# Performance work log

Hardware: AMD Instinct MI355X
Metric: run time of the kernel (lower is better)

Reference implementation:

```python
import jax, jax.numpy as jnp
import numpy as np

ALPHA = 0.2  # LeakyReLU negative slope

def setup_inputs() -> dict:
    key = jax.random.key(0)
    k1, k2, k3 = jax.random.split(key, 3)
    B, N, IN_DIM = 16, 1024, 128
    HEADS, HEAD_DIM = 2, 64  # out_dim = 128
    h = jax.random.normal(k1, (B, N, IN_DIM), dtype=jnp.float32)
    # xavier_uniform with gain=1.414 ~ uniform(-b, b); exact init unimportant for correctness
    bW = 1.414 * np.sqrt(6.0 / (IN_DIM + HEAD_DIM))
    W = jax.random.uniform(k2, (HEADS, IN_DIM, HEAD_DIM), minval=-bW, maxval=bW, dtype=jnp.float32)
    ba = 1.414 * np.sqrt(6.0 / (2 * HEAD_DIM + 1))
    a = jax.random.uniform(k3, (HEADS, 2 * HEAD_DIM, 1), minval=-ba, maxval=ba, dtype=jnp.float32)
    return {"h": h, "W": W, "a": a}

def reference(h, W, a):
    B, N, in_dim = h.shape
    heads, _, head_dim = W.shape
    out_dim = heads * head_dim
    # h_prime: [B, N, H, D]
    hp = jnp.einsum('bni,hio->bnho', h, W)
    # Split additive attention: a . [h_i ; h_j] = a_src . h_i + a_dst . h_j (same math as concat)
    a_src = a[:, :head_dim, 0]   # [H, D]
    a_dst = a[:, head_dim:, 0]   # [H, D]
    e_src = jnp.einsum('bnhd,hd->bhn', hp, a_src)  # [B, H, N]
    e_dst = jnp.einsum('bmhd,hd->bhm', hp, a_dst)  # [B, H, N]
    e = e_src[:, :, :, None] + e_dst[:, :, None, :]  # [B, H, N, N]
    e = jnp.where(e >= 0, e, ALPHA * e)  # LeakyReLU(0.2)
    att = jax.nn.softmax(e, axis=-1)
    # dropout p=0.0 (eval-deterministic): no-op
    h_new = jnp.einsum('bhnm,bmho->bnho', att, hp).reshape(B, N, out_dim)
    out = h_new + h if in_dim == out_dim else h_new
    return jax.nn.elu(out)
```

## Files before the change

kernel.cpp:

```cpp
#include <hip/hip_runtime.h>
#include <math.h>


#define LOG2E 1.44269504088896340736f

typedef __bf16 bf16x8 __attribute__((ext_vector_type(8)));
typedef float floatx4 __attribute__((ext_vector_type(4)));

union U16x8 { uint4 u; bf16x8 b; };

__device__ __forceinline__ unsigned short f2bf(float f) {
    union { __bf16 b; unsigned short u; } x;
    x.b = (__bf16)f;
    return x.u;
}

__global__ __launch_bounds__(256) void gat_prep(
    const float* __restrict__ Wg,
    const float* __restrict__ ag,
    unsigned short* __restrict__ Wp,
    float* __restrict__ acat)
{
    const int t = threadIdx.x;
    const int base = blockIdx.x * 1024;
#pragma unroll
    for (int i = 0; i < 4; ++i) {
        int idx = base + i * 256 + t;
        int c = idx & 127, k = idx >> 7;
        float v = Wg[(c >> 6) * 8192 + k * 64 + (c & 63)];
        Wp[((k >> 3) * 128 + c) * 8 + (k & 7)] = f2bf(v);
    }
    if (blockIdx.x == 0 && t < 128) {
        acat[t]       = ag[(t >> 6) * 128 + (t & 63)];
        acat[128 + t] = ag[(t >> 6) * 128 + 64 + (t & 63)];
    }
}

__global__ __launch_bounds__(256) void gat_hp(
    const float* __restrict__ hg,
    const unsigned short* __restrict__ Wp,
    const float* __restrict__ acat,
    unsigned short* __restrict__ hpB,
    float* __restrict__ es_g,
    float* __restrict__ ed_g)
{
    const int t = threadIdx.x;
    const int lane = t & 63;
    const int wv = blockIdx.x * 4 + (t >> 6);
    const int rt = wv >> 1;
    const int half = wv & 1;
    const int n0 = rt * 16;
    const int col = lane & 15, quad = lane >> 4;

    floatx4 acc[4];
#pragma unroll
    for (int ct = 0; ct < 4; ++ct) acc[ct] = (floatx4){0.f, 0.f, 0.f, 0.f};

    const float* hrow = hg + (size_t)(n0 + col) * 128;
    const uint4* wp4 = (const uint4*)Wp;
#pragma unroll
    for (int kq = 0; kq < 4; ++kq) {
        float4 h0 = *(const float4*)(hrow + kq * 32 + quad * 8);
        float4 h1 = *(const float4*)(hrow + kq * 32 + quad * 8 + 4);
        bf16x8 af;
        af[0] = (__bf16)h0.x; af[1] = (__bf16)h0.y;
        af[2] = (__bf16)h0.z; af[3] = (__bf16)h0.w;
        af[4] = (__bf16)h1.x; af[5] = (__bf16)h1.y;
        af[6] = (__bf16)h1.z; af[7] = (__bf16)h1.w;
        const uint4* wbase = wp4 + (size_t)(kq * 4 + quad) * 128 + half * 64;
#pragma unroll
        for (int ct = 0; ct < 4; ++ct) {
            U16x8 bu; bu.u = wbase[ct * 16 + col];
            acc[ct] = __builtin_amdgcn_mfma_f32_16x16x32_bf16(af, bu.b, acc[ct], 0, 0, 0);
        }
    }

    const int b = n0 >> 10;
    const int nloc = n0 & 1023;
    const int bh = b * 2 + half;

    float esr[4] = {0.f, 0.f, 0.f, 0.f}, edr[4] = {0.f, 0.f, 0.f, 0.f};
#pragma unroll
    for (int ct = 0; ct < 4; ++ct) {
        int c = half * 64 + ct * 16 + col;
        float as = acat[c], ad = acat[128 + c];
#pragma unroll
        for (int r = 0; r < 4; ++r) {
            esr[r] = fmaf(acc[ct][r], as, esr[r]);
            edr[r] = fmaf(acc[ct][r], ad, edr[r]);
        }
    }
#pragma unroll
    for (int off = 1; off <= 8; off <<= 1) {
#pragma unroll
        for (int r = 0; r < 4; ++r) {
            esr[r] += __shfl_xor(esr[r], off, 64);
            edr[r] += __shfl_xor(edr[r], off, 64);
        }
    }
    if (col == 0) {
        size_t base = (size_t)bh * 1024 + nloc + quad * 4;
#pragma unroll
        for (int r = 0; r < 4; ++r) {
            es_g[base + r] = esr[r];
            ed_g[base + r] = edr[r];
        }
    }

    const int gloc = (nloc >> 3) + (quad >> 1);
#pragma unroll
    for (int ct = 0; ct < 4; ++ct) {
        int d = ct * 16 + col;
        uint2 pk;
        pk.x = (unsigned)f2bf(acc[ct][0]) | ((unsigned)f2bf(acc[ct][1]) << 16);
        pk.y = (unsigned)f2bf(acc[ct][2]) | ((unsigned)f2bf(acc[ct][3]) << 16);
        size_t idx = ((size_t)(bh * 128 + gloc) * 64 + d) * 8 + (quad & 1) * 4;
        *(uint2*)(hpB + idx) = pk;
    }
}

__global__ __launch_bounds__(256, 4) void gat_attn(
    const float* __restrict__ hg,
    const unsigned short* __restrict__ hpB,
    const float* __restrict__ es_g,
    const float* __restrict__ ed_g,
    float* __restrict__ out)
{
    __shared__ float red[4 * 64 * 17];

    const int t = threadIdx.x;
    const int lane = t & 63;
    const int w = t >> 6;
    const int bh = blockIdx.x & 31;
    const int nt = blockIdx.x >> 5;
    const int b = bh >> 1, hh = bh & 1;
    const int n0 = nt * 16;
    const int col = lane & 15, quad = lane >> 4;

    const float* edrow = ed_g + (size_t)bh * 1024;

    float mx = -1e30f;
#pragma unroll
    for (int i = 0; i < 4; ++i) {
        float4 v = *(const float4*)(edrow + lane * 16 + i * 4);
        mx = fmaxf(mx, fmaxf(fmaxf(v.x, v.y), fmaxf(v.z, v.w)));
    }
#pragma unroll
    for (int off = 1; off < 64; off <<= 1) mx = fmaxf(mx, __shfl_xor(mx, off, 64));

    const float s2 = es_g[(size_t)bh * 1024 + n0 + col] * LOG2E;
    const float x0 = s2 + mx * LOG2E;
    const float M = fmaxf(x0, 0.2f * x0);
    const float s2m = s2 - M;
    const float s5m = 0.2f * s2 - M;
    const float K = LOG2E, K5 = 0.2f * LOG2E;

    floatx4 acc[4];
#pragma unroll
    for (int ct = 0; ct < 4; ++ct) acc[ct] = (floatx4){0.f, 0.f, 0.f, 0.f};
    float lsum = 0.f;

    const uint4* hb = (const uint4*)hpB + (size_t)bh * 8192;
    const int mbase = w * 256;

    float4 d0 = *(const float4*)(edrow + mbase + quad * 8);
    float4 d1 = *(const float4*)(edrow + mbase + quad * 8 + 4);
    int gm = (mbase >> 3) + quad;
    uint4 bu0 = hb[gm * 64 + col];
    uint4 bu1 = hb[gm * 64 + 16 + col];
    uint4 bu2 = hb[gm * 64 + 32 + col];
    uint4 bu3 = hb[gm * 64 + 48 + col];

#pragma unroll
    for (int i = 0; i < 8; ++i) {
        float4 c0 = d0, c1 = d1;
        uint4 cb0 = bu0, cb1 = bu1, cb2 = bu2, cb3 = bu3;
        if (i < 7) {
            int m1 = mbase + (i + 1) * 32;
            d0 = *(const float4*)(edrow + m1 + quad * 8);
            d1 = *(const float4*)(edrow + m1 + quad * 8 + 4);
            gm = (m1 >> 3) + quad;
            bu0 = hb[gm * 64 + col];
            bu1 = hb[gm * 64 + 16 + col];
            bu2 = hb[gm * 64 + 32 + col];
            bu3 = hb[gm * 64 + 48 + col];
        }
        float dv[8] = {c0.x, c0.y, c0.z, c0.w, c1.x, c1.y, c1.z, c1.w};
        bf16x8 af;
#pragma unroll
        for (int j = 0; j < 8; ++j) {
            float a1 = fmaf(dv[j], K, s2m);
            float a2 = fmaf(dv[j], K5, s5m);
            float p = __builtin_amdgcn_exp2f(fmaxf(a1, a2));
            lsum += p;
            af[j] = (__bf16)p;
        }
        U16x8 u0; u0.u = cb0;
        U16x8 u1; u1.u = cb1;
        U16x8 u2; u2.u = cb2;
        U16x8 u3; u3.u = cb3;
        acc[0] = __builtin_amdgcn_mfma_f32_16x16x32_bf16(af, u0.b, acc[0], 0, 0, 0);
        acc[1] = __builtin_amdgcn_mfma_f32_16x16x32_bf16(af, u1.b, acc[1], 0, 0, 0);
        acc[2] = __builtin_amdgcn_mfma_f32_16x16x32_bf16(af, u2.b, acc[2], 0, 0, 0);
        acc[3] = __builtin_amdgcn_mfma_f32_16x16x32_bf16(af, u3.b, acc[3], 0, 0, 0);
    }

    lsum += __shfl_xor(lsum, 16, 64);
    lsum += __shfl_xor(lsum, 32, 64);

    float* myred = red + (w * 64 + lane) * 17;
#pragma unroll
    for (int ct = 0; ct < 4; ++ct)
#pragma unroll
        for (int r = 0; r < 4; ++r) myred[ct * 4 + r] = acc[ct][r];
    myred[16] = lsum;
    __syncthreads();

    float facc[4] = {0.f, 0.f, 0.f, 0.f};
    float ltot = 0.f;
#pragma unroll
    for (int v = 0; v < 4; ++v) {
        const float* rr = red + (v * 64 + lane) * 17;
#pragma unroll
        for (int r = 0; r < 4; ++r) facc[r] += rr[w * 4 + r];
        ltot += rr[16];
    }
    float inv[4];
#pragma unroll
    for (int r = 0; r < 4; ++r)
        inv[r] = __builtin_amdgcn_rcpf(__shfl(ltot, quad * 4 + r, 16));

#pragma unroll
    for (int r = 0; r < 4; ++r) {
        int n = n0 + quad * 4 + r;
        size_t off = (size_t)(b * 1024 + n) * 128 + hh * 64 + w * 16 + col;
        float v = facc[r] * inv[r] + hg[off];
        out[off] = v > 0.f ? v : __builtin_amdgcn_exp2f(v * LOG2E) - 1.f;
    }
}

extern "C" void kernel_launch(void* const* d_in, const int* in_sizes, int n_in,
                              void* d_out, int out_size, void* d_ws, size_t ws_size,
                              hipStream_t stream) {
    const float* h = (const float*)d_in[0];
    const float* W = (const float*)d_in[1];
    const float* a = (const float*)d_in[2];
    float* out = (float*)d_out;

    unsigned short* hpB = (unsigned short*)d_ws;
    float* es  = (float*)((char*)d_ws + (4u << 20));
    float* ed  = es + 32 * 1024;
    unsigned short* Wp = (unsigned short*)(ed + 32 * 1024);
    float* acat = (float*)((char*)Wp + 16384 * sizeof(unsigned short));

    gat_prep<<<16, 256, 0, stream>>>(W, a, Wp, acat);
    gat_hp<<<512, 256, 0, stream>>>(h, Wp, acat, hpB, es, ed);
    gat_attn<<<2048, 256, 0, stream>>>(h, hpB, es, ed, out);
}
```

Before: 86.57 us.

## Fuse weight prep into projection kernel and double query rows per attention block

The separate weight-conversion kernel is removed. Each projection block now converts W to bf16 into shared memory itself and reads the attention vector directly, which drops one launch and its dependency. The attention kernel now handles 32 query rows per block instead of 16, reusing each loaded hp tile for two MFMA accumulator sets and halving the grid. In exchange, every projection block redoes the W conversion, and the attention kernel uses more registers and a larger shared reduction buffer, which may lower occupancy.

Result: slower. 104.6 us (+20.8%).

```diff
diff --git a/kernel.cpp b/kernel.cpp
--- a/kernel.cpp
+++ b/kernel.cpp
@@ -15,49 +15,44 @@
     return x.u;
 }
 
-__global__ __launch_bounds__(256) void gat_prep(
+__global__ __launch_bounds__(256) void gat_hp(
+    const float* __restrict__ hg,
     const float* __restrict__ Wg,
     const float* __restrict__ ag,
-    unsigned short* __restrict__ Wp,
-    float* __restrict__ acat)
-{
-    const int t = threadIdx.x;
-    const int base = blockIdx.x * 1024;
-#pragma unroll
-    for (int i = 0; i < 4; ++i) {
-        int idx = base + i * 256 + t;
-        int c = idx & 127, k = idx >> 7;
-        float v = Wg[(c >> 6) * 8192 + k * 64 + (c & 63)];
-        Wp[((k >> 3) * 128 + c) * 8 + (k & 7)] = f2bf(v);
-    }
-    if (blockIdx.x == 0 && t < 128) {
-        acat[t]       = ag[(t >> 6) * 128 + (t & 63)];
-        acat[128 + t] = ag[(t >> 6) * 128 + 64 + (t & 63)];
-    }
-}
-
-__global__ __launch_bounds__(256) void gat_hp(
-    const float* __restrict__ hg,
-    const unsigned short* __restrict__ Wp,
-    const float* __restrict__ acat,
     unsigned short* __restrict__ hpB,
     float* __restrict__ es_g,
     float* __restrict__ ed_g)
 {
+    __shared__ unsigned short wp[16 * 128 * 8];
+
     const int t = threadIdx.x;
     const int lane = t & 63;
+    const int col = lane & 15, quad = lane >> 4;
+
+#pragma unroll
+    for (int i = 0; i < 16; ++i) {
+        int lin = (i * 256 + t) * 4;
+        int head = lin >> 13, k = (lin >> 6) & 127, d = lin & 63;
+        float4 v = *(const float4*)(Wg + lin);
+        int base = ((k >> 3) * 128 + head * 64 + d) * 8 + (k & 7);
+        wp[base]      = f2bf(v.x);
+        wp[base + 8]  = f2bf(v.y);
+        wp[base + 16] = f2bf(v.z);
+        wp[base + 24] = f2bf(v.w);
+    }
+    __syncthreads();
+
     const int wv = blockIdx.x * 4 + (t >> 6);
     const int rt = wv >> 1;
     const int half = wv & 1;
     const int n0 = rt * 16;
-    const int col = lane & 15, quad = lane >> 4;
 
     floatx4 acc[4];
 #pragma unroll
     for (int ct = 0; ct < 4; ++ct) acc[ct] = (floatx4){0.f, 0.f, 0.f, 0.f};
 
     const float* hrow = hg + (size_t)(n0 + col) * 128;
-    const uint4* wp4 = (const uint4*)Wp;
+    const uint4* wl = (const uint4*)wp;
 #pragma unroll
     for (int kq = 0; kq < 4; ++kq) {
         float4 h0 = *(const float4*)(hrow + kq * 32 + quad * 8);
@@ -67,10 +62,10 @@
         af[2] = (__bf16)h0.z; af[3] = (__bf16)h0.w;
         af[4] = (__bf16)h1.x; af[5] = (__bf16)h1.y;
         af[6] = (__bf16)h1.z; af[7] = (__bf16)h1.w;
-        const uint4* wbase = wp4 + (size_t)(kq * 4 + quad) * 128 + half * 64;
+        const int u = (kq * 4 + quad) * 128 + half * 64;
 #pragma unroll
         for (int ct = 0; ct < 4; ++ct) {
-            U16x8 bu; bu.u = wbase[ct * 16 + col];
+            U16x8 bu; bu.u = wl[u + ct * 16 + col];
             acc[ct] = __builtin_amdgcn_mfma_f32_16x16x32_bf16(af, bu.b, acc[ct], 0, 0, 0);
         }
     }
@@ -82,8 +77,9 @@
     float esr[4] = {0.f, 0.f, 0.f, 0.f}, edr[4] = {0.f, 0.f, 0.f, 0.f};
 #pragma unroll
     for (int ct = 0; ct < 4; ++ct) {
-        int c = half * 64 + ct * 16 + col;
-        float as = acat[c], ad = acat[128 + c];
+        int d = ct * 16 + col;
+        float as = ag[half * 128 + d];
+        float ad = ag[half * 128 + 64 + d];
 #pragma unroll
         for (int r = 0; r < 4; ++r) {
             esr[r] = fmaf(acc[ct][r], as, esr[r]);
@@ -119,14 +115,14 @@
     }
 }
 
-__global__ __launch_bounds__(256, 4) void gat_attn(
+__global__ __launch_bounds__(256, 4) void gat_att(
     const float* __restrict__ hg,
     const unsigned short* __restrict__ hpB,
     const float* __restrict__ es_g,
     const float* __restrict__ ed_g,
     float* __restrict__ out)
 {
-    __shared__ float red[4 * 64 * 17];
+    __shared__ float red[4 * 64 * 35];
 
     const int t = threadIdx.x;
     const int lane = t & 63;
@@ -134,7 +130,7 @@
     const int bh = blockIdx.x & 31;
     const int nt = blockIdx.x >> 5;
     const int b = bh >> 1, hh = bh & 1;
-    const int n0 = nt * 16;
+    const int n0 = nt * 32;
     const int col = lane & 15, quad = lane >> 4;
 
     const float* edrow = ed_g + (size_t)bh * 1024;
@@ -147,18 +143,23 @@
     }
 #pragma unroll
     for (int off = 1; off < 64; off <<= 1) mx = fmaxf(mx, __shfl_xor(mx, off, 64));
-
-    const float s2 = es_g[(size_t)bh * 1024 + n0 + col] * LOG2E;
-    const float x0 = s2 + mx * LOG2E;
-    const float M = fmaxf(x0, 0.2f * x0);
-    const float s2m = s2 - M;
-    const float s5m = 0.2f * s2 - M;
+    const float mxl = mx * LOG2E;
+
+    const float s2a = es_g[(size_t)bh * 1024 + n0 + col] * LOG2E;
+    const float s2b = es_g[(size_t)bh * 1024 + n0 + 16 + col] * LOG2E;
+    const float x0a = s2a + mxl, x0b = s2b + mxl;
+    const float Ma = fmaxf(x0a, 0.2f * x0a), Mb = fmaxf(x0b, 0.2f * x0b);
+    const float s2ma = s2a - Ma, s5ma = 0.2f * s2a - Ma;
+    const float s2mb = s2b - Mb, s5mb = 0.2f * s2b - Mb;
     const float K = LOG2E, K5 = 0.2f * LOG2E;
 
-    floatx4 acc[4];
-#pragma unroll
-    for (int ct = 0; ct < 4; ++ct) acc[ct] = (floatx4){0.f, 0.f, 0.f, 0.f};
-    float lsum = 0.f;
+    floatx4 acc0[4], acc1[4];
+#pragma unroll
+    for (int ct = 0; ct < 4; ++ct) {
+        acc0[ct] = (floatx4){0.f, 0.f, 0.f, 0.f};
+        acc1[ct] = (floatx4){0.f, 0.f, 0.f, 0.f};
+    }
+    float ls0 = 0.f, ls1 = 0.f;
 
     const uint4* hb = (const uint4*)hpB + (size_t)bh * 8192;
     const int mbase = w * 256;
@@ -186,56 +187,72 @@
             bu3 = hb[gm * 64 + 48 + col];
         }
         float dv[8] = {c0.x, c0.y, c0.z, c0.w, c1.x, c1.y, c1.z, c1.w};
-        bf16x8 af;
+        bf16x8 af0, af1;
 #pragma unroll
         for (int j = 0; j < 8; ++j) {
-            float a1 = fmaf(dv[j], K, s2m);
-            float a2 = fmaf(dv[j], K5, s5m);
-            float p = __builtin_amdgcn_exp2f(fmaxf(a1, a2));
-            lsum += p;
-            af[j] = (__bf16)p;
+            float pa = __builtin_amdgcn_exp2f(fmaxf(fmaf(dv[j], K, s2ma), fmaf(dv[j], K5, s5ma)));
+            float pb = __builtin_amdgcn_exp2f(fmaxf(fmaf(dv[j], K, s2mb), fmaf(dv[j], K5, s5mb)));
+            ls0 += pa; ls1 += pb;
+            af0[j] = (__bf16)pa;
+            af1[j] = (__bf16)pb;
         }
         U16x8 u0; u0.u = cb0;
         U16x8 u1; u1.u = cb1;
         U16x8 u2; u2.u = cb2;
         U16x8 u3; u3.u = cb3;
-        acc[0] = __builtin_amdgcn_mfma_f32_16x16x32_bf16(af, u0.b, acc[0], 0, 0, 0);
-        acc[1] = __builtin_amdgcn_mfma_f32_16x16x32_bf16(af, u1.b, acc[1], 0, 0, 0);
-        acc[2] = __builtin_amdgcn_mfma_f32_16x16x32_bf16(af, u2.b, acc[2], 0, 0, 0);
-        acc[3] = __builtin_amdgcn_mfma_f32_16x16x32_bf16(af, u3.b, acc[3], 0, 0, 0);
-    }
-
-    lsum += __shfl_xor(lsum, 16, 64);
-    lsum += __shfl_xor(lsum, 32, 64);
-
-    float* myred = red + (w * 64 + lane) * 17;
+        acc0[0] = __builtin_amdgcn_mfma_f32_16x16x32_bf16(af0, u0.b, acc0[0], 0, 0, 0);
+        acc1[0] = __builtin_amdgcn_mfma_f32_16x16x32_bf16(af1, u0.b, acc1[0], 0, 0, 0);
+        acc0[1] = __builtin_amdgcn_mfma_f32_16x16x32_bf16(af0, u1.b, acc0[1], 0, 0, 0);
+        acc1[1] = __builtin_amdgcn_mfma_f32_16x16x32_bf16(af1, u1.b, acc1[1], 0, 0, 0);
+        acc0[2] = __builtin_amdgcn_mfma_f32_16x16x32_bf16(af0, u2.b, acc0[2], 0, 0, 0);
+        acc1[2] = __builtin_amdgcn_mfma_f32_16x16x32_bf16(af1, u2.b, acc1[2], 0, 0, 0);
+        acc0[3] = __builtin_amdgcn_mfma_f32_16x16x32_bf16(af0, u3.b, acc0[3], 0, 0, 0);
+        acc1[3] = __builtin_amdgcn_mfma_f32_16x16x32_bf16(af1, u3.b, acc1[3], 0, 0, 0);
+    }
+
+    ls0 += __shfl_xor(ls0, 16, 64); ls0 += __shfl_xor(ls0, 32, 64);
+    ls1 += __shfl_xor(ls1, 16, 64); ls1 += __shfl_xor(ls1, 32, 64);
+
+    float* myred = red + (w * 64 + lane) * 35;
 #pragma unroll
     for (int ct = 0; ct < 4; ++ct)
 #pragma unroll
-        for (int r = 0; r < 4; ++r) myred[ct * 4 + r] = acc[ct][r];
-    myred[16] = lsum;
+        for (int r = 0; r < 4; ++r) {
+            myred[ct * 4 + r]      = acc0[ct][r];
+            myred[16 + ct * 4 + r] = acc1[ct][r];
+        }
+    myred[32] = ls0;
+    myred[33] = ls1;
     __syncthreads();
 
-    float facc[4] = {0.f, 0.f, 0.f, 0.f};
+    const int tile = w & 1;
+    const int ctp = w >> 1;
     float ltot = 0.f;
 #pragma unroll
-    for (int v = 0; v < 4; ++v) {
-        const float* rr = red + (v * 64 + lane) * 17;
-#pragma unroll
-        for (int r = 0; r < 4; ++r) facc[r] += rr[w * 4 + r];
-        ltot += rr[16];
-    }
+    for (int v4 = 0; v4 < 4; ++v4)
+        ltot += red[(v4 * 64 + lane) * 35 + 32 + tile];
     float inv[4];
 #pragma unroll
     for (int r = 0; r < 4; ++r)
         inv[r] = __builtin_amdgcn_rcpf(__shfl(ltot, quad * 4 + r, 16));
 
 #pragma unroll
-    for (int r = 0; r < 4; ++r) {
-        int n = n0 + quad * 4 + r;
-        size_t off = (size_t)(b * 1024 + n) * 128 + hh * 64 + w * 16 + col;
-        float v = facc[r] * inv[r] + hg[off];
-        out[off] = v > 0.f ? v : __builtin_amdgcn_exp2f(v * LOG2E) - 1.f;
+    for (int cti = 0; cti < 2; ++cti) {
+        const int ct = ctp * 2 + cti;
+        float facc[4] = {0.f, 0.f, 0.f, 0.f};
+#pragma unroll
+        for (int v4 = 0; v4 < 4; ++v4) {
+            const float* rr = red + (v4 * 64 + lane) * 35 + tile * 16 + ct * 4;
+#pragma unroll
+            for (int r = 0; r < 4; ++r) facc[r] += rr[r];
+        }
+#pragma unroll
+        for (int r = 0; r < 4; ++r) {
+            int n = n0 + tile * 16 + quad * 4 + r;
+            size_t off = (size_t)(b * 1024 + n) * 128 + hh * 64 + ct * 16 + col;
+            float vv = facc[r] * inv[r] + hg[off];
+            out[off] = vv > 0.f ? vv : __builtin_amdgcn_exp2f(vv * LOG2E) - 1.f;
+        }
     }
 }
 
@@ -250,10 +267,7 @@
     unsigned short* hpB = (unsigned short*)d_ws;
     float* es  = (float*)((char*)d_ws + (4u << 20));
     float* ed  = es + 32 * 1024;
-    unsigned short* Wp = (unsigned short*)(ed + 32 * 1024);
-    float* acat = (float*)((char*)Wp + 16384 * sizeof(unsigned short));
-
-    gat_prep<<<16, 256, 0, stream>>>(W, a, Wp, acat);
-    gat_hp<<<512, 256, 0, stream>>>(h, Wp, acat, hpB, es, ed);
-    gat_attn<<<2048, 256, 0, stream>>>(h, hpB, es, ed, out);
-}
+
+    gat_hp<<<512, 256, 0, stream>>>(h, W, a, hpB, es, ed);
+    gat_att<<<1024, 256, 0, stream>>>(h, hpB, es, ed, out);
+}
```
